# Kernel tuning notes

Measured on AMD Instinct MI355X. Metric: run time of the kernel, lower is better.

Reference implementation:

```python
import jax, jax.numpy as jnp
import numpy as np

EPS = 1e-8  # torch F.cosine_similarity eps


def _gather(features, idx):
    # batched_index_select_tensor: per-batch gather along seq dim
    return jnp.take_along_axis(features, idx[:, :, None], axis=1)


def setup_inputs() -> dict:
    key = jax.random.key(0)
    ks = jax.random.split(key, 7)
    B, S, H, Q, D, C = 8, 512, 768, 64, 256, 2
    return {
        "features": jax.random.normal(ks[0], (B, S, H), dtype=jnp.float32),
        "text_a_indices": jax.random.randint(ks[1], (B, Q), 0, S),
        "text_b_indices": jax.random.randint(ks[2], (B, D), 0, S),
        "W1": jax.random.normal(ks[3], (2 * H, H), dtype=jnp.float32) * 0.02,
        "b1": jax.random.normal(ks[4], (H,), dtype=jnp.float32) * 0.02,
        "W2": jax.random.normal(ks[5], (H, C), dtype=jnp.float32) * 0.02,
        "b2": jax.random.normal(ks[6], (C,), dtype=jnp.float32) * 0.02,
    }


def reference(features, text_a_indices, text_b_indices, W1, b1, W2, b2):
    dt = features.dtype
    a_mask = (text_a_indices > 0).astype(dt)          # [B,Q]
    b_mask = (text_b_indices > 0).astype(dt)          # [B,D]
    a_len = jnp.sum(a_mask, axis=-1)                  # [B]
    b_len = jnp.sum(b_mask, axis=-1)                  # [B]

    q_vec = _gather(features, text_a_indices)         # [B,Q,H]
    d_vec = _gather(features, text_b_indices)         # [B,D,H]

    # cosine similarity with torch eps semantics: x.y / (max(|x|,eps)*max(|y|,eps))
    qn = q_vec / jnp.maximum(jnp.linalg.norm(q_vec, axis=-1, keepdims=True), EPS)
    dn = d_vec / jnp.maximum(jnp.linalg.norm(d_vec, axis=-1, keepdims=True), EPS)
    sim = jnp.einsum("bqh,bdh->bqd", qn, dn)          # [B,Q,D]

    # masked weighted average over doc tokens, per query token (fused; no 4D repeat)
    sim_m = sim * b_mask[:, None, :]
    per_q_doc = jnp.einsum("bqd,bdh->bqh", sim_m, d_vec) / b_len[:, None, None]

    # masked average over query tokens
    am = a_mask[:, :, None]
    query_based_doc = jnp.sum(per_q_doc * am, axis=1) / a_len[:, None]   # [B,H]
    query_avg = jnp.sum(q_vec * am, axis=1) / a_len[:, None]             # [B,H]

    feat = jnp.concatenate([query_avg, query_based_doc], axis=-1)        # [B,2H]
    hidden = jax.nn.relu(feat @ W1 + b1)
    logits = hidden @ W2 + b2
    return logits
```

## Files before the change

### kernel.cpp

```cpp
#include <hip/hip_runtime.h>
#include <hip/hip_bf16.h>

#define B_ 8
#define S_ 512
#define H_ 768
#define Q_ 64
#define D_ 256
#define EPSF 1e-8f

#define WS_INVD   0
#define WS_QBARP  (B_ * D_)
#define WS_QAP    (WS_QBARP + 2 * B_ * H_)
#define WS_W      (WS_QAP + 2 * B_ * H_)
#define WS_HIDDEN (WS_W + B_ * D_)
#define WS_CNT    (WS_HIDDEN + B_ * H_)

__global__ __launch_bounds__(512) void k_pre(
        const float* __restrict__ feats,
        const int* __restrict__ aidx,
        const int* __restrict__ bidx,
        float* __restrict__ ws) {
    float* invd      = ws + WS_INVD;
    float* qbar_part = ws + WS_QBARP;
    float* qa_part   = ws + WS_QAP;
    const int t = threadIdx.x, wv = t >> 6, lane = t & 63;

    if (blockIdx.x < 192) {
        const int b = blockIdx.x / 24, rem = blockIdx.x % 24;
        const int hc = rem >> 1, qg = rem & 1;
        __shared__ int   s_ai[32];
        __shared__ float s_inv[32], s_m[32];
        __shared__ float red0[8][64], red1[8][64];
        if (t < 32) s_ai[t] = aidx[b * Q_ + qg * 32 + t];
        __syncthreads();
#pragma unroll
        for (int j = 0; j < 4; ++j) {
            int q = wv * 4 + j;
            int idx = s_ai[q];
            const float4* row4 = (const float4*)(feats + (size_t)(b * S_ + idx) * H_);
            float4 v0 = row4[lane], v1 = row4[lane + 64], v2 = row4[lane + 128];
            float ss = v0.x*v0.x + v0.y*v0.y + v0.z*v0.z + v0.w*v0.w
                     + v1.x*v1.x + v1.y*v1.y + v1.z*v1.z + v1.w*v1.w
                     + v2.x*v2.x + v2.y*v2.y + v2.z*v2.z + v2.w*v2.w;
            for (int off = 32; off; off >>= 1) ss += __shfl_xor(ss, off, 64);
            if (lane == 0) {
                float inv = 1.f / fmaxf(sqrtf(ss), EPSF);
                s_inv[q] = (idx > 0) ? inv : 0.f;
                s_m[q]   = (idx > 0) ? 1.f : 0.f;
            }
        }
        __syncthreads();
        int h = hc * 64 + lane;
        float pb = 0.f, pa = 0.f;
#pragma unroll
        for (int j = 0; j < 4; ++j) {
            int q = wv * 4 + j;
            const float* row = feats + (size_t)(b * S_ + s_ai[q]) * H_;
            float f = row[h];
            pb += f * s_inv[q];
            pa += f * s_m[q];
        }
        red0[wv][lane] = pb;
        red1[wv][lane] = pa;
        __syncthreads();
        if (t < 64) {
            float sb = 0.f, sa = 0.f;
#pragma unroll
            for (int k = 0; k < 8; ++k) { sb += red0[k][t]; sa += red1[k][t]; }
            qbar_part[(size_t)(qg * B_ + b) * H_ + hc * 64 + t] = sb;
            qa_part[(size_t)(qg * B_ + b) * H_ + hc * 64 + t]   = sa;
        }
    } else {
        int gw = (blockIdx.x - 192) * 8 + wv;
#pragma unroll
        for (int j = 0; j < 4; ++j) {
            int g = gw * 4 + j;
            int b = g >> 8, d = g & 255;
            int idx = bidx[b * D_ + d];
            const float4* row4 = (const float4*)(feats + (size_t)(b * S_ + idx) * H_);
            float4 v0 = row4[lane], v1 = row4[lane + 64], v2 = row4[lane + 128];
            float ss = v0.x*v0.x + v0.y*v0.y + v0.z*v0.z + v0.w*v0.w
                     + v1.x*v1.x + v1.y*v1.y + v1.z*v1.z + v1.w*v1.w
                     + v2.x*v2.x + v2.y*v2.y + v2.z*v2.z + v2.w*v2.w;
            for (int off = 32; off; off >>= 1) ss += __shfl_xor(ss, off, 64);
            if (lane == 0)
                invd[b * D_ + d] = (idx > 0) ? 1.f / fmaxf(sqrtf(ss), EPSF) : 0.f;
        }
    }
}

__global__ __launch_bounds__(256) void k_docw(
        const float* __restrict__ feats,
        const int* __restrict__ aidx,
        const int* __restrict__ bidx,
        float* __restrict__ ws) {
    const float* invd      = ws + WS_INVD;
    const float* qbar_part = ws + WS_QBARP;
    float* w               = ws + WS_W;
    float* zero_region     = ws + WS_HIDDEN;
    const int t = threadIdx.x, wv = t >> 6, lane = t & 63;
    if (blockIdx.x < 25) zero_region[blockIdx.x * 256 + t] = 0.f;
    int gw = blockIdx.x * 4 + wv;
    int b = gw >> 8, d = gw & 255;
    __shared__ int cnt[4];
    __shared__ float s_alen;
    unsigned long long mb = __ballot(bidx[b * D_ + wv * 64 + lane] > 0);
    if (lane == 0) cnt[wv] = __popcll(mb);
    if (wv == 0) {
        unsigned long long ma = __ballot(aidx[b * Q_ + lane] > 0);
        if (lane == 0) s_alen = (float)__popcll(ma);
    }
    __syncthreads();
    float blen = (float)(cnt[0] + cnt[1] + cnt[2] + cnt[3]);
    int idx = bidx[b * D_ + d];
    const float4* row4 = (const float4*)(feats + (size_t)(b * S_ + idx) * H_);
    const float4* q0 = (const float4*)(qbar_part + (size_t)b * H_);
    const float4* q1 = (const float4*)(qbar_part + (size_t)(B_ + b) * H_);
    float dqf = 0.f;
#pragma unroll
    for (int k = 0; k < 3; ++k) {
        float4 v  = row4[lane + k * 64];
        float4 qa = q0[lane + k * 64];
        float4 qb = q1[lane + k * 64];
        dqf += v.x * (qa.x + qb.x) + v.y * (qa.y + qb.y)
             + v.z * (qa.z + qb.z) + v.w * (qa.w + qb.w);
    }
    for (int off = 32; off; off >>= 1) dqf += __shfl_xor(dqf, off, 64);
    if (lane == 0)
        w[b * D_ + d] = dqf * invd[b * D_ + d] / (s_alen * blen);
}

__global__ __launch_bounds__(256) void k_docsum_mlp(
        const float* __restrict__ feats,
        const int* __restrict__ aidx,
        const int* __restrict__ bidx,
        const float* __restrict__ W1,
        const float* __restrict__ b1,
        const float* __restrict__ W2,
        const float* __restrict__ b2,
        float* __restrict__ ws,
        float* __restrict__ out) {
    const float* qa_part = ws + WS_QAP;
    const float* w       = ws + WS_W;
    float* hidden        = ws + WS_HIDDEN;
    int* counter         = (int*)(ws + WS_CNT);
    const int b = blockIdx.x / 12, hc = blockIdx.x % 12;
    const int t = threadIdx.x, wv = t >> 6, lane = t & 63;
    __shared__ float s_w[D_];
    __shared__ int   s_i[D_];
    __shared__ float s_k[128];
    __shared__ float red[4][64];
    __shared__ float s_alen;
    __shared__ int   s_flag;
    s_w[t] = w[b * D_ + t];
    s_i[t] = bidx[b * D_ + t];
    if (wv == 0) {
        unsigned long long ma = __ballot(aidx[b * Q_ + lane] > 0);
        if (lane == 0) s_alen = (float)__popcll(ma);
    }
    __syncthreads();
    if (t < 64) {
        s_k[t] = (qa_part[(size_t)b * H_ + hc * 64 + t]
                + qa_part[(size_t)(B_ + b) * H_ + hc * 64 + t]) / s_alen;
    }
    int hh = hc * 64 + lane;
    float acc = 0.f;
#pragma unroll 8
    for (int d = wv * 64; d < wv * 64 + 64; ++d)
        acc += s_w[d] * feats[(size_t)(b * S_ + s_i[d]) * H_ + hh];
    red[wv][lane] = acc;
    __syncthreads();
    if (t < 64) s_k[64 + t] = red[0][t] + red[1][t] + red[2][t] + red[3][t];
    __syncthreads();
    const float* Wtop = W1 + (size_t)(hc * 64) * H_;
    const float* Wbot = W1 + (size_t)(H_ + hc * 64) * H_;
    float h0 = 0.f, h1 = 0.f, h2 = 0.f;
#pragma unroll 4
    for (int i = 0; i < 64; ++i) {
        float ka = s_k[i], kb = s_k[64 + i];
        const float* r1 = Wtop + (size_t)i * H_;
        const float* r2 = Wbot + (size_t)i * H_;
        h0 += ka * r1[t]       + kb * r2[t];
        h1 += ka * r1[t + 256] + kb * r2[t + 256];
        h2 += ka * r1[t + 512] + kb * r2[t + 512];
    }
    atomicAdd(&hidden[b * H_ + t],       h0);
    atomicAdd(&hidden[b * H_ + t + 256], h1);
    atomicAdd(&hidden[b * H_ + t + 512], h2);
    __threadfence();
    __syncthreads();
    if (t == 0) {
        int old = atomicAdd(counter, 1);
        s_flag = (old == 95);
    }
    __syncthreads();
    if (s_flag) {
        __threadfence();
        for (int bb = wv * 2; bb < wv * 2 + 2; ++bb) {
            float a0 = 0.f, a1 = 0.f;
#pragma unroll
            for (int k = 0; k < 12; ++k) {
                int h = lane + k * 64;
                float hv = __hip_atomic_load(&hidden[bb * H_ + h],
                                             __ATOMIC_RELAXED,
                                             __HIP_MEMORY_SCOPE_AGENT);
                float v = fmaxf(hv + b1[h], 0.f);
                a0 += v * W2[h * 2 + 0];
                a1 += v * W2[h * 2 + 1];
            }
            for (int off = 32; off; off >>= 1) {
                a0 += __shfl_xor(a0, off, 64);
                a1 += __shfl_xor(a1, off, 64);
            }
            if (lane == 0) {
                out[bb * 2 + 0] = a0 + b2[0];
                out[bb * 2 + 1] = a1 + b2[1];
            }
        }
    }
}

extern "C" void kernel_launch(void* const* d_in, const int* in_sizes, int n_in,
                              void* d_out, int out_size, void* d_ws, size_t ws_size,
                              hipStream_t stream) {
    const float* feats = (const float*)d_in[0];
    const int*   aidx  = (const int*)d_in[1];
    const int*   bidx  = (const int*)d_in[2];
    const float* W1    = (const float*)d_in[3];
    const float* b1    = (const float*)d_in[4];
    const float* W2    = (const float*)d_in[5];
    const float* b2    = (const float*)d_in[6];
    float* out = (float*)d_out;
    float* ws = (float*)d_ws;

    k_pre<<<256, 512, 0, stream>>>(feats, aidx, bidx, ws);
    k_docw<<<512, 256, 0, stream>>>(feats, aidx, bidx, ws);
    k_docsum_mlp<<<96, 256, 0, stream>>>(feats, aidx, bidx, W1, b1, W2, b2, ws, out);
}
```

Measured before the change: 102.9 us.

## Fuse doc-norm computation into doc-weight kernel and repartition query partial sums

Doc token norms are now computed inside the doc-weight kernel from the same row it already loads, so the separate doc-norm pass and its extra gather over doc rows go away. The query pass is restructured into 64 blocks, each reducing 8 query rows over the full hidden dimension, which produces 8 partial sums that the later kernels add up. The doc-weight kernel stages the summed query vector in shared memory, so each block now re-reads 8 partials, and the first kernel runs with fewer blocks.

```diff
diff --git a/kernel.cpp b/kernel.cpp
--- a/kernel.cpp
+++ b/kernel.cpp
@@ -8,84 +8,57 @@
 #define D_ 256
 #define EPSF 1e-8f
 
-#define WS_INVD   0
-#define WS_QBARP  (B_ * D_)
-#define WS_QAP    (WS_QBARP + 2 * B_ * H_)
-#define WS_W      (WS_QAP + 2 * B_ * H_)
-#define WS_HIDDEN (WS_W + B_ * D_)
+#define WS_QBARP  0
+#define WS_QAP    (8 * B_ * H_)
+#define WS_W      (16 * B_ * H_)
+#define WS_HIDDEN (16 * B_ * H_ + B_ * D_)
 #define WS_CNT    (WS_HIDDEN + B_ * H_)
 
-__global__ __launch_bounds__(512) void k_pre(
+__global__ __launch_bounds__(512) void k_qnorm(
         const float* __restrict__ feats,
         const int* __restrict__ aidx,
-        const int* __restrict__ bidx,
         float* __restrict__ ws) {
-    float* invd      = ws + WS_INVD;
     float* qbar_part = ws + WS_QBARP;
     float* qa_part   = ws + WS_QAP;
+    const int b = blockIdx.x >> 3, qg = blockIdx.x & 7;
     const int t = threadIdx.x, wv = t >> 6, lane = t & 63;
-
-    if (blockIdx.x < 192) {
-        const int b = blockIdx.x / 24, rem = blockIdx.x % 24;
-        const int hc = rem >> 1, qg = rem & 1;
-        __shared__ int   s_ai[32];
-        __shared__ float s_inv[32], s_m[32];
-        __shared__ float red0[8][64], red1[8][64];
-        if (t < 32) s_ai[t] = aidx[b * Q_ + qg * 32 + t];
-        __syncthreads();
-#pragma unroll
-        for (int j = 0; j < 4; ++j) {
-            int q = wv * 4 + j;
-            int idx = s_ai[q];
-            const float4* row4 = (const float4*)(feats + (size_t)(b * S_ + idx) * H_);
-            float4 v0 = row4[lane], v1 = row4[lane + 64], v2 = row4[lane + 128];
-            float ss = v0.x*v0.x + v0.y*v0.y + v0.z*v0.z + v0.w*v0.w
-                     + v1.x*v1.x + v1.y*v1.y + v1.z*v1.z + v1.w*v1.w
-                     + v2.x*v2.x + v2.y*v2.y + v2.z*v2.z + v2.w*v2.w;
-            for (int off = 32; off; off >>= 1) ss += __shfl_xor(ss, off, 64);
-            if (lane == 0) {
-                float inv = 1.f / fmaxf(sqrtf(ss), EPSF);
-                s_inv[q] = (idx > 0) ? inv : 0.f;
-                s_m[q]   = (idx > 0) ? 1.f : 0.f;
-            }
+    __shared__ int   s_ai[8];
+    __shared__ float s_inv[8], s_m[8];
+    if (t < 8) s_ai[t] = aidx[b * Q_ + qg * 8 + t];
+    __syncthreads();
+    {
+        int idx = s_ai[wv];
+        const float4* row4 = (const float4*)(feats + (size_t)(b * S_ + idx) * H_);
+        float4 v0 = row4[lane], v1 = row4[lane + 64], v2 = row4[lane + 128];
+        float ss = v0.x*v0.x + v0.y*v0.y + v0.z*v0.z + v0.w*v0.w
+                 + v1.x*v1.x + v1.y*v1.y + v1.z*v1.z + v1.w*v1.w
+                 + v2.x*v2.x + v2.y*v2.y + v2.z*v2.z + v2.w*v2.w;
+        for (int off = 32; off; off >>= 1) ss += __shfl_xor(ss, off, 64);
+        if (lane == 0) {
+            float inv = 1.f / fmaxf(sqrtf(ss), EPSF);
+            s_inv[wv] = (idx > 0) ? inv : 0.f;
+            s_m[wv]   = (idx > 0) ? 1.f : 0.f;
         }
-        __syncthreads();
-        int h = hc * 64 + lane;
-        float pb = 0.f, pa = 0.f;
-#pragma unroll
-        for (int j = 0; j < 4; ++j) {
-            int q = wv * 4 + j;
-            const float* row = feats + (size_t)(b * S_ + s_ai[q]) * H_;
-            float f = row[h];
-            pb += f * s_inv[q];
-            pa += f * s_m[q];
+    }
+    __syncthreads();
+    float pb0 = 0.f, pa0 = 0.f, pb1 = 0.f, pa1 = 0.f;
+#pragma unroll
+    for (int j = 0; j < 8; ++j) {
+        const float* row = feats + (size_t)(b * S_ + s_ai[j]) * H_;
+        float iv = s_inv[j], mv = s_m[j];
+        float f0 = row[t];
+        pb0 += f0 * iv; pa0 += f0 * mv;
+        if (t < 256) {
+            float f1 = row[512 + t];
+            pb1 += f1 * iv; pa1 += f1 * mv;
         }
-        red0[wv][lane] = pb;
-        red1[wv][lane] = pa;
-        __syncthreads();
-        if (t < 64) {
-            float sb = 0.f, sa = 0.f;
-#pragma unroll
-            for (int k = 0; k < 8; ++k) { sb += red0[k][t]; sa += red1[k][t]; }
-            qbar_part[(size_t)(qg * B_ + b) * H_ + hc * 64 + t] = sb;
-            qa_part[(size_t)(qg * B_ + b) * H_ + hc * 64 + t]   = sa;
-        }
-    } else {
-        int gw = (blockIdx.x - 192) * 8 + wv;
-#pragma unroll
-        for (int j = 0; j < 4; ++j) {
-            int g = gw * 4 + j;
-            int b = g >> 8, d = g & 255;
-            int idx = bidx[b * D_ + d];
-            const float4* row4 = (const float4*)(feats + (size_t)(b * S_ + idx) * H_);
-            float4 v0 = row4[lane], v1 = row4[lane + 64], v2 = row4[lane + 128];
-            float ss = v0.x*v0.x + v0.y*v0.y + v0.z*v0.z + v0.w*v0.w
-                     + v1.x*v1.x + v1.y*v1.y + v1.z*v1.z + v1.w*v1.w
-                     + v2.x*v2.x + v2.y*v2.y + v2.z*v2.z + v2.w*v2.w;
-            for (int off = 32; off; off >>= 1) ss += __shfl_xor(ss, off, 64);
-            if (lane == 0)
-                invd[b * D_ + d] = (idx > 0) ? 1.f / fmaxf(sqrtf(ss), EPSF) : 0.f;
-        }
+    }
+    size_t base = (size_t)(qg * B_ + b) * H_;
+    qbar_part[base + t] = pb0;
+    qa_part[base + t]   = pa0;
+    if (t < 256) {
+        qbar_part[base + 512 + t] = pb1;
+        qa_part[base + 512 + t]   = pa1;
     }
 }
 
@@ -94,16 +67,25 @@
         const int* __restrict__ aidx,
         const int* __restrict__ bidx,
         float* __restrict__ ws) {
-    const float* invd      = ws + WS_INVD;
     const float* qbar_part = ws + WS_QBARP;
-    float* w               = ws + WS_W;
-    float* zero_region     = ws + WS_HIDDEN;
+    float* w           = ws + WS_W;
+    float* zero_region = ws + WS_HIDDEN;
     const int t = threadIdx.x, wv = t >> 6, lane = t & 63;
     if (blockIdx.x < 25) zero_region[blockIdx.x * 256 + t] = 0.f;
-    int gw = blockIdx.x * 4 + wv;
-    int b = gw >> 8, d = gw & 255;
+    const int gw = blockIdx.x * 4 + wv;
+    const int b = gw >> 8, d = gw & 255;
+    __shared__ __align__(16) float s_qbar[H_];
     __shared__ int cnt[4];
     __shared__ float s_alen;
+#pragma unroll
+    for (int c = 0; c < 3; ++c) {
+        int col = c * 256 + t;
+        float s = 0.f;
+#pragma unroll
+        for (int p = 0; p < 8; ++p)
+            s += qbar_part[(size_t)(p * B_ + b) * H_ + col];
+        s_qbar[col] = s;
+    }
     unsigned long long mb = __ballot(bidx[b * D_ + wv * 64 + lane] > 0);
     if (lane == 0) cnt[wv] = __popcll(mb);
     if (wv == 0) {
@@ -114,20 +96,24 @@
     float blen = (float)(cnt[0] + cnt[1] + cnt[2] + cnt[3]);
     int idx = bidx[b * D_ + d];
     const float4* row4 = (const float4*)(feats + (size_t)(b * S_ + idx) * H_);
-    const float4* q0 = (const float4*)(qbar_part + (size_t)b * H_);
-    const float4* q1 = (const float4*)(qbar_part + (size_t)(B_ + b) * H_);
-    float dqf = 0.f;
+    const float4* q4 = (const float4*)s_qbar;
+    float dqf = 0.f, dff = 0.f;
 #pragma unroll
     for (int k = 0; k < 3; ++k) {
-        float4 v  = row4[lane + k * 64];
-        float4 qa = q0[lane + k * 64];
-        float4 qb = q1[lane + k * 64];
-        dqf += v.x * (qa.x + qb.x) + v.y * (qa.y + qb.y)
-             + v.z * (qa.z + qb.z) + v.w * (qa.w + qb.w);
-    }
-    for (int off = 32; off; off >>= 1) dqf += __shfl_xor(dqf, off, 64);
-    if (lane == 0)
-        w[b * D_ + d] = dqf * invd[b * D_ + d] / (s_alen * blen);
+        float4 v = row4[lane + k * 64];
+        float4 q = q4[lane + k * 64];
+        dqf += v.x*q.x + v.y*q.y + v.z*q.z + v.w*q.w;
+        dff += v.x*v.x + v.y*v.y + v.z*v.z + v.w*v.w;
+    }
+    for (int off = 32; off; off >>= 1) {
+        dqf += __shfl_xor(dqf, off, 64);
+        dff += __shfl_xor(dff, off, 64);
+    }
+    if (lane == 0) {
+        float invd = 1.f / fmaxf(sqrtf(dff), EPSF);
+        float scale = 1.f / (s_alen * blen);
+        w[b * D_ + d] = (idx > 0) ? dqf * invd * scale : 0.f;
+    }
 }
 
 __global__ __launch_bounds__(256) void k_docsum_mlp(
@@ -160,8 +146,11 @@
     }
     __syncthreads();
     if (t < 64) {
-        s_k[t] = (qa_part[(size_t)b * H_ + hc * 64 + t]
-                + qa_part[(size_t)(B_ + b) * H_ + hc * 64 + t]) / s_alen;
+        float s = 0.f;
+#pragma unroll
+        for (int p = 0; p < 8; ++p)
+            s += qa_part[(size_t)(p * B_ + b) * H_ + hc * 64 + t];
+        s_k[t] = s / s_alen;
     }
     int hh = hc * 64 + lane;
     float acc = 0.f;
@@ -233,7 +222,7 @@
     float* out = (float*)d_out;
     float* ws = (float*)d_ws;
 
-    k_pre<<<256, 512, 0, stream>>>(feats, aidx, bidx, ws);
+    k_qnorm<<<64, 512, 0, stream>>>(feats, aidx, ws);
     k_docw<<<512, 256, 0, stream>>>(feats, aidx, bidx, ws);
     k_docsum_mlp<<<96, 256, 0, stream>>>(feats, aidx, bidx, W1, b1, W2, b2, ws, out);
 }
```

Measured after the change: 101.9 us. Within noise of the previous version (-1.0%).
